# Kernel tuning notes

Measured on AMD Instinct MI355X. Metric: run time of the kernel, lower is better.

Reference implementation:

```python
import jax, jax.numpy as jnp
import numpy as np

B, D, N_CAT, S = 8192, 128, 8192, 4
EPS = 1e-12  # F.normalize eps


def setup_inputs() -> dict:
    key = jax.random.key(0)
    k1, k2, k3, k4 = jax.random.split(key, 4)
    return {
        "batch_x": jax.random.normal(k1, (B, D), dtype=jnp.float32),
        "cat": jax.random.normal(k2, (N_CAT, D), dtype=jnp.float32),
        "y": jax.random.uniform(k3, (N_CAT,), dtype=jnp.float32),
        "phi": jax.random.normal(k4, (S, D), dtype=jnp.float32) * (6.0 / (D + 1)) ** 0.5,  # xavier-ish scale
        "bias": jnp.zeros((1,), dtype=jnp.float32),
    }


def reference(batch_x, cat, y, phi, bias):
    # con[n, b] = cat[n] . batch_x[b]   -> [N_cat, B]
    con = cat @ batch_x.T
    # F.normalize(con, p=4, dim=0): divide each column by its 4-norm (clamped)
    norm4 = jnp.sum(jnp.abs(con) ** 4, axis=0, keepdims=True) ** 0.25
    con = con / jnp.maximum(norm4, EPS)
    con = jax.nn.softmax(con, axis=0)
    s = phi.shape[0]
    c = con.shape[0] // s
    psi = con.reshape(s, c, con.shape[1])      # source_size chunks of [C, B]
    y_r = y.reshape(s, c)                      # source_size chunks of labels
    theta = jnp.exp(batch_x @ phi.T).T         # [S, B], raw exp (theta/sum_src unused in original)
    # sum over sources and chunk rows of y[s,c] * psi[s,c,b] * theta[s,b]
    y_hat = jnp.einsum('sc,scb,sb->b', y_r, psi, theta) + bias
    return y_hat
```

## Files before the change

kernel.cpp:

```cpp
#include <hip/hip_runtime.h>
#include <hip/hip_bf16.h>
#include <math.h>

typedef __bf16 bf16x8 __attribute__((ext_vector_type(8)));
typedef float f32x4 __attribute__((ext_vector_type(4)));

namespace {
constexpr int BN   = 8192;
constexpr int DK   = 128;
constexpr int NCAT = 8192;
constexpr int SRC  = 4;
constexpr int RG   = 8;
constexpr int LDK  = 136;
}

__device__ __forceinline__ float4 ld4(const float* p) {
    return *reinterpret_cast<const float4*>(p);
}

__global__ __launch_bounds__(256) void k_convert(const float* __restrict__ in,
                                                 unsigned short* __restrict__ out,
                                                 int n8) {
    const int i = blockIdx.x * 256 + threadIdx.x;
    if (i >= n8) return;
    const float4 a = ld4(in + (size_t)i * 8);
    const float4 b = ld4(in + (size_t)i * 8 + 4);
    float vals[8] = {a.x, a.y, a.z, a.w, b.x, b.y, b.z, b.w};
    union { unsigned short u[8]; uint4 v; } o;
#pragma unroll
    for (int j = 0; j < 8; ++j) {
        __hip_bfloat16 h = __float2bfloat16(vals[j]);
        o.u[j] = *reinterpret_cast<unsigned short*>(&h);
    }
    *reinterpret_cast<uint4*>(&out[(size_t)i * 8]) = o.v;
}

template <int PASS>
__global__ __launch_bounds__(256, 2) void k_mfma_pass(
    const unsigned short* __restrict__ xb,
    const unsigned short* __restrict__ catb,
    const float* __restrict__ y,
    const float* __restrict__ inv_norm,
    const float* __restrict__ vmax,
    float* __restrict__ outA,
    float* __restrict__ outB) {
    __shared__ __align__(16) unsigned short As[128 * LDK];
    __shared__ __align__(16) unsigned short Bs[128 * LDK];
    __shared__ float ysh[128];
    __shared__ float redA[2][128];
    __shared__ float redB[2][128];

    const int t = threadIdx.x;
    const int colbase = blockIdx.x * 128;
    const int rowgrp = blockIdx.y;
    const int rowbase0 = rowgrp * 1024;

    const int wid = t >> 6;
    const int lane = t & 63;
    const int wr = wid >> 1;
    const int wc = wid & 1;
    const int lr = lane & 15;
    const int kb = lane >> 4;

#pragma unroll
    for (int q = t; q < 2048; q += 256) {
        const int c = q >> 4, kc = q & 15;
        *reinterpret_cast<uint4*>(&Bs[c * LDK + kc * 8]) =
            *reinterpret_cast<const uint4*>(&xb[(size_t)(colbase + c) * DK + kc * 8]);
    }

    float accA[4], accB[4];
    float inm[4], vmx4[4];
#pragma unroll
    for (int j = 0; j < 4; ++j) {
        accA[j] = 0.f;
        accB[j] = (PASS == 1) ? -3.0e38f : 0.f;
        if (PASS == 2) {
            const int col = colbase + wc * 64 + j * 16 + lr;
            inm[j] = inv_norm[col];
            vmx4[j] = vmax[col];
        }
    }

    for (int rt = 0; rt < 8; ++rt) {
        const int rowbase = rowbase0 + rt * 128;
        __syncthreads();
#pragma unroll
        for (int q = t; q < 2048; q += 256) {
            const int r = q >> 4, kc = q & 15;
            *reinterpret_cast<uint4*>(&As[r * LDK + kc * 8]) =
                *reinterpret_cast<const uint4*>(&catb[(size_t)(rowbase + r) * DK + kc * 8]);
        }
        if (PASS == 2 && t < 128) ysh[t] = y[rowbase + t];
        __syncthreads();

        f32x4 acc[4][4];
#pragma unroll
        for (int i = 0; i < 4; ++i)
#pragma unroll
            for (int j = 0; j < 4; ++j) acc[i][j] = (f32x4){0.f, 0.f, 0.f, 0.f};

#pragma unroll
        for (int kk = 0; kk < 4; ++kk) {
            bf16x8 a[4], b[4];
#pragma unroll
            for (int i = 0; i < 4; ++i)
                a[i] = *reinterpret_cast<const bf16x8*>(
                    &As[(wr * 64 + i * 16 + lr) * LDK + kk * 32 + kb * 8]);
#pragma unroll
            for (int j = 0; j < 4; ++j)
                b[j] = *reinterpret_cast<const bf16x8*>(
                    &Bs[(wc * 64 + j * 16 + lr) * LDK + kk * 32 + kb * 8]);
#pragma unroll
            for (int i = 0; i < 4; ++i)
#pragma unroll
                for (int j = 0; j < 4; ++j)
                    acc[i][j] = __builtin_amdgcn_mfma_f32_16x16x32_bf16(
                        a[i], b[j], acc[i][j], 0, 0, 0);
        }

        if (PASS == 1) {
#pragma unroll
            for (int i = 0; i < 4; ++i)
#pragma unroll
                for (int j = 0; j < 4; ++j)
#pragma unroll
                    for (int r = 0; r < 4; ++r) {
                        const float v = acc[i][j][r];
                        const float v2 = v * v;
                        accA[j] += v2 * v2;
                        accB[j] = fmaxf(accB[j], v);
                    }
        } else {
#pragma unroll
            for (int i = 0; i < 4; ++i)
#pragma unroll
                for (int r = 0; r < 4; ++r) {
                    const float yr = ysh[wr * 64 + i * 16 + kb * 4 + r];
#pragma unroll
                    for (int j = 0; j < 4; ++j) {
                        const float e = __expf(fmaf(acc[i][j][r], inm[j], -vmx4[j]));
                        accA[j] += e;
                        accB[j] += yr * e;
                    }
                }
        }
    }

#pragma unroll
    for (int j = 0; j < 4; ++j) {
        float a16 = __shfl_xor(accA[j], 16, 64);
        float b16 = __shfl_xor(accB[j], 16, 64);
        accA[j] += a16;
        accB[j] = (PASS == 1) ? fmaxf(accB[j], b16) : accB[j] + b16;
        float a32 = __shfl_xor(accA[j], 32, 64);
        float b32 = __shfl_xor(accB[j], 32, 64);
        accA[j] += a32;
        accB[j] = (PASS == 1) ? fmaxf(accB[j], b32) : accB[j] + b32;
    }

    if (lane < 16) {
#pragma unroll
        for (int j = 0; j < 4; ++j) {
            redA[wr][wc * 64 + j * 16 + lane] = accA[j];
            redB[wr][wc * 64 + j * 16 + lane] = accB[j];
        }
    }
    __syncthreads();
    if (t < 128) {
        const float a = redA[0][t] + redA[1][t];
        const float b = (PASS == 1) ? fmaxf(redB[0][t], redB[1][t])
                                    : redB[0][t] + redB[1][t];
        outA[(size_t)rowgrp * BN + colbase + t] = a;
        outB[(size_t)rowgrp * BN + colbase + t] = b;
    }
}

__global__ __launch_bounds__(256) void k_norm(const float* __restrict__ pp4,
                                              const float* __restrict__ pmax,
                                              float* __restrict__ inv_norm,
                                              float* __restrict__ vmax) {
    const int b = blockIdx.x * 256 + threadIdx.x;
    float sp = 0.f, sm = -3.0e38f;
#pragma unroll
    for (int r = 0; r < RG; ++r) {
        sp += pp4[r * BN + b];
        sm = fmaxf(sm, pmax[r * BN + b]);
    }
    float n4 = sqrtf(sqrtf(sp));
    n4 = fmaxf(n4, 1e-12f);
    const float inv = 1.0f / n4;
    inv_norm[b] = inv;
    vmax[b] = sm * inv;
}

__global__ __launch_bounds__(256) void k_final(const float* __restrict__ x,
                                               const float* __restrict__ phi,
                                               const float* __restrict__ pZ,
                                               const float* __restrict__ pW,
                                               const float* __restrict__ bias,
                                               float* __restrict__ out) {
    const int g = blockIdx.x * 256 + threadIdx.x;
    const int b = g >> 2, s = g & 3;
    float dot = 0.f;
#pragma unroll
    for (int k = 0; k < DK; k += 4) {
        const float4 xv = ld4(&x[(size_t)b * DK + k]);
        const float4 pv = ld4(&phi[s * DK + k]);
        dot += xv.x * pv.x + xv.y * pv.y + xv.z * pv.z + xv.w * pv.w;
    }
    const float W = pW[(size_t)(2 * s) * BN + b] + pW[(size_t)(2 * s + 1) * BN + b];
    float v = __expf(dot) * W;
    float Z = pZ[(size_t)(2 * s) * BN + b] + pZ[(size_t)(2 * s + 1) * BN + b];
    v += __shfl_xor(v, 1, 64);
    v += __shfl_xor(v, 2, 64);
    Z += __shfl_xor(Z, 1, 64);
    Z += __shfl_xor(Z, 2, 64);
    if (s == 0) out[b] = v / Z + bias[0];
}

extern "C" void kernel_launch(void* const* d_in, const int* in_sizes, int n_in,
                              void* d_out, int out_size, void* d_ws, size_t ws_size,
                              hipStream_t stream) {
    const float* x    = (const float*)d_in[0];
    const float* cat  = (const float*)d_in[1];
    const float* y    = (const float*)d_in[2];
    const float* phi  = (const float*)d_in[3];
    const float* bias = (const float*)d_in[4];
    float* out = (float*)d_out;

    char* ws = (char*)d_ws;
    unsigned short* xb   = (unsigned short*)ws;
    unsigned short* catb = xb + (size_t)BN * DK;
    float* pp4      = (float*)(catb + (size_t)NCAT * DK);
    float* pmax     = pp4 + (size_t)RG * BN;
    float* inv_norm = pmax + (size_t)RG * BN;
    float* vmax     = inv_norm + BN;
    float* pZ       = vmax + BN;
    float* pW       = pZ + (size_t)RG * BN;

    k_convert<<<(BN * DK / 8 + 255) / 256, 256, 0, stream>>>(x, xb, BN * DK / 8);
    k_convert<<<(NCAT * DK / 8 + 255) / 256, 256, 0, stream>>>(cat, catb, NCAT * DK / 8);
    k_mfma_pass<1><<<dim3(BN / 128, RG), 256, 0, stream>>>(xb, catb, y, nullptr, nullptr,
                                                           pp4, pmax);
    k_norm<<<BN / 256, 256, 0, stream>>>(pp4, pmax, inv_norm, vmax);
    k_mfma_pass<2><<<dim3(BN / 128, RG), 256, 0, stream>>>(xb, catb, y, inv_norm, vmax,
                                                           pZ, pW);
    k_final<<<BN * SRC / 256, 256, 0, stream>>>(x, phi, pZ, pW, bias, out);
}
```

Before: 73.76 us.

## Keep x tile in registers, fuse norm kernel and converts, use exp2

Loads the x (B operand) fragments straight into registers once per block instead of staging them in LDS, and doubles the cat row tile to 256 rows. The A tile alone then occupies LDS. Merges the two conversion launches into one and folds the separate norm kernel into the start of pass 2, with log2e pre-multiplied so exp2f replaces __expf. This cuts launch count, LDS traffic and LDS footprint, at the cost of extra registers for the persistent B fragments, which could affect the 2-blocks-per-CU occupancy.

```diff
diff --git a/kernel.cpp b/kernel.cpp
--- a/kernel.cpp
+++ b/kernel.cpp
@@ -12,41 +12,50 @@
 constexpr int SRC  = 4;
 constexpr int RG   = 8;
 constexpr int LDK  = 136;
+constexpr int RT   = 256;
+constexpr float LOG2E = 1.4426950408889634f;
 }
 
 __device__ __forceinline__ float4 ld4(const float* p) {
     return *reinterpret_cast<const float4*>(p);
 }
 
-__global__ __launch_bounds__(256) void k_convert(const float* __restrict__ in,
-                                                 unsigned short* __restrict__ out,
-                                                 int n8) {
+__global__ __launch_bounds__(256) void k_convert2(const float* __restrict__ x,
+                                                  const float* __restrict__ cat,
+                                                  unsigned short* __restrict__ xb,
+                                                  unsigned short* __restrict__ catb) {
     const int i = blockIdx.x * 256 + threadIdx.x;
-    if (i >= n8) return;
-    const float4 a = ld4(in + (size_t)i * 8);
-    const float4 b = ld4(in + (size_t)i * 8 + 4);
+    const int nx = BN * DK / 8;
+    const float* src;
+    unsigned short* dst;
+    int j;
+    if (i < nx) { src = x; dst = xb; j = i; }
+    else        { src = cat; dst = catb; j = i - nx; }
+    const float4 a = ld4(src + (size_t)j * 8);
+    const float4 b = ld4(src + (size_t)j * 8 + 4);
     float vals[8] = {a.x, a.y, a.z, a.w, b.x, b.y, b.z, b.w};
     union { unsigned short u[8]; uint4 v; } o;
 #pragma unroll
-    for (int j = 0; j < 8; ++j) {
-        __hip_bfloat16 h = __float2bfloat16(vals[j]);
-        o.u[j] = *reinterpret_cast<unsigned short*>(&h);
-    }
-    *reinterpret_cast<uint4*>(&out[(size_t)i * 8]) = o.v;
+    for (int q = 0; q < 8; ++q) {
+        __hip_bfloat16 h = __float2bfloat16(vals[q]);
+        o.u[q] = *reinterpret_cast<unsigned short*>(&h);
+    }
+    *reinterpret_cast<uint4*>(&dst[(size_t)j * 8]) = o.v;
 }
 
 template <int PASS>
-__global__ __launch_bounds__(256, 2) void k_mfma_pass(
+__global__ __launch_bounds__(256, 2) void k_pass(
     const unsigned short* __restrict__ xb,
     const unsigned short* __restrict__ catb,
     const float* __restrict__ y,
-    const float* __restrict__ inv_norm,
-    const float* __restrict__ vmax,
+    const float* __restrict__ pp4,
+    const float* __restrict__ pmax,
     float* __restrict__ outA,
     float* __restrict__ outB) {
-    __shared__ __align__(16) unsigned short As[128 * LDK];
-    __shared__ __align__(16) unsigned short Bs[128 * LDK];
-    __shared__ float ysh[128];
+    __shared__ __align__(16) unsigned short As[RT * LDK];
+    __shared__ float ysh[RT];
+    __shared__ float nsh[128];
+    __shared__ float msh[128];
     __shared__ float redA[2][128];
     __shared__ float redB[2][128];
 
@@ -62,88 +71,105 @@
     const int lr = lane & 15;
     const int kb = lane >> 4;
 
-#pragma unroll
-    for (int q = t; q < 2048; q += 256) {
-        const int c = q >> 4, kc = q & 15;
-        *reinterpret_cast<uint4*>(&Bs[c * LDK + kc * 8]) =
-            *reinterpret_cast<const uint4*>(&xb[(size_t)(colbase + c) * DK + kc * 8]);
+    if (PASS == 2 && t < 128) {
+        float sp = 0.f, sm = -3.0e38f;
+#pragma unroll
+        for (int r = 0; r < RG; ++r) {
+            sp += pp4[r * BN + colbase + t];
+            sm = fmaxf(sm, pmax[r * BN + colbase + t]);
+        }
+        const float n4 = fmaxf(sqrtf(sqrtf(sp)), 1e-12f);
+        const float L = LOG2E / n4;
+        nsh[t] = L;
+        msh[t] = sm * L;
+    }
+
+    bf16x8 Bf[4][4];
+#pragma unroll
+    for (int j = 0; j < 4; ++j)
+#pragma unroll
+        for (int kk = 0; kk < 4; ++kk)
+            Bf[j][kk] = *reinterpret_cast<const bf16x8*>(
+                &xb[(size_t)(colbase + wc * 64 + j * 16 + lr) * DK + kk * 32 + kb * 8]);
+
+    float inm[4], vmx4[4];
+    if (PASS == 2) {
+        __syncthreads();
+#pragma unroll
+        for (int j = 0; j < 4; ++j) {
+            inm[j] = nsh[wc * 64 + j * 16 + lr];
+            vmx4[j] = msh[wc * 64 + j * 16 + lr];
+        }
     }
 
     float accA[4], accB[4];
-    float inm[4], vmx4[4];
 #pragma unroll
     for (int j = 0; j < 4; ++j) {
         accA[j] = 0.f;
         accB[j] = (PASS == 1) ? -3.0e38f : 0.f;
-        if (PASS == 2) {
-            const int col = colbase + wc * 64 + j * 16 + lr;
-            inm[j] = inv_norm[col];
-            vmx4[j] = vmax[col];
-        }
-    }
-
-    for (int rt = 0; rt < 8; ++rt) {
-        const int rowbase = rowbase0 + rt * 128;
+    }
+
+    for (int rt0 = 0; rt0 < 1024; rt0 += RT) {
+        const int rowbase = rowbase0 + rt0;
         __syncthreads();
 #pragma unroll
-        for (int q = t; q < 2048; q += 256) {
+        for (int q = t; q < RT * 16; q += 256) {
             const int r = q >> 4, kc = q & 15;
             *reinterpret_cast<uint4*>(&As[r * LDK + kc * 8]) =
                 *reinterpret_cast<const uint4*>(&catb[(size_t)(rowbase + r) * DK + kc * 8]);
         }
-        if (PASS == 2 && t < 128) ysh[t] = y[rowbase + t];
+        if (PASS == 2) ysh[t] = y[rowbase + t];
         __syncthreads();
 
-        f32x4 acc[4][4];
-#pragma unroll
-        for (int i = 0; i < 4; ++i)
-#pragma unroll
-            for (int j = 0; j < 4; ++j) acc[i][j] = (f32x4){0.f, 0.f, 0.f, 0.f};
-
-#pragma unroll
-        for (int kk = 0; kk < 4; ++kk) {
-            bf16x8 a[4], b[4];
+#pragma unroll
+        for (int ch = 0; ch < 2; ++ch) {
+            f32x4 acc[4][4];
 #pragma unroll
             for (int i = 0; i < 4; ++i)
-                a[i] = *reinterpret_cast<const bf16x8*>(
-                    &As[(wr * 64 + i * 16 + lr) * LDK + kk * 32 + kb * 8]);
-#pragma unroll
-            for (int j = 0; j < 4; ++j)
-                b[j] = *reinterpret_cast<const bf16x8*>(
-                    &Bs[(wc * 64 + j * 16 + lr) * LDK + kk * 32 + kb * 8]);
-#pragma unroll
-            for (int i = 0; i < 4; ++i)
-#pragma unroll
-                for (int j = 0; j < 4; ++j)
-                    acc[i][j] = __builtin_amdgcn_mfma_f32_16x16x32_bf16(
-                        a[i], b[j], acc[i][j], 0, 0, 0);
-        }
-
-        if (PASS == 1) {
-#pragma unroll
-            for (int i = 0; i < 4; ++i)
-#pragma unroll
-                for (int j = 0; j < 4; ++j)
+#pragma unroll
+                for (int j = 0; j < 4; ++j) acc[i][j] = (f32x4){0.f, 0.f, 0.f, 0.f};
+
+#pragma unroll
+            for (int kk = 0; kk < 4; ++kk) {
+                bf16x8 a[4];
+#pragma unroll
+                for (int i = 0; i < 4; ++i)
+                    a[i] = *reinterpret_cast<const bf16x8*>(
+                        &As[(ch * 128 + wr * 64 + i * 16 + lr) * LDK + kk * 32 + kb * 8]);
+#pragma unroll
+                for (int i = 0; i < 4; ++i)
+#pragma unroll
+                    for (int j = 0; j < 4; ++j)
+                        acc[i][j] = __builtin_amdgcn_mfma_f32_16x16x32_bf16(
+                            a[i], Bf[j][kk], acc[i][j], 0, 0, 0);
+            }
+
+            if (PASS == 1) {
+#pragma unroll
+                for (int i = 0; i < 4; ++i)
+#pragma unroll
+                    for (int j = 0; j < 4; ++j)
+#pragma unroll
+                        for (int r = 0; r < 4; ++r) {
+                            const float v = acc[i][j][r];
+                            const float v2 = v * v;
+                            accA[j] = fmaf(v2, v2, accA[j]);
+                            accB[j] = fmaxf(accB[j], v);
+                        }
+            } else {
+#pragma unroll
+                for (int i = 0; i < 4; ++i)
 #pragma unroll
                     for (int r = 0; r < 4; ++r) {
-                        const float v = acc[i][j][r];
-                        const float v2 = v * v;
-                        accA[j] += v2 * v2;
-                        accB[j] = fmaxf(accB[j], v);
+                        const float yr = ysh[ch * 128 + wr * 64 + i * 16 + kb * 4 + r];
+#pragma unroll
+                        for (int j = 0; j < 4; ++j) {
+                            const float e = exp2f(fmaf(acc[i][j][r], inm[j], -vmx4[j]));
+                            accA[j] += e;
+                            accB[j] = fmaf(yr, e, accB[j]);
+                        }
                     }
-        } else {
-#pragma unroll
-            for (int i = 0; i < 4; ++i)
-#pragma unroll
-                for (int r = 0; r < 4; ++r) {
-                    const float yr = ysh[wr * 64 + i * 16 + kb * 4 + r];
-#pragma unroll
-                    for (int j = 0; j < 4; ++j) {
-                        const float e = __expf(fmaf(acc[i][j][r], inm[j], -vmx4[j]));
-                        accA[j] += e;
-                        accB[j] += yr * e;
-                    }
-                }
+            }
         }
     }
 
@@ -176,24 +202,6 @@
     }
 }
 
-__global__ __launch_bounds__(256) void k_norm(const float* __restrict__ pp4,
-                                              const float* __restrict__ pmax,
-                                              float* __restrict__ inv_norm,
-                                              float* __restrict__ vmax) {
-    const int b = blockIdx.x * 256 + threadIdx.x;
-    float sp = 0.f, sm = -3.0e38f;
-#pragma unroll
-    for (int r = 0; r < RG; ++r) {
-        sp += pp4[r * BN + b];
-        sm = fmaxf(sm, pmax[r * BN + b]);
-    }
-    float n4 = sqrtf(sqrtf(sp));
-    n4 = fmaxf(n4, 1e-12f);
-    const float inv = 1.0f / n4;
-    inv_norm[b] = inv;
-    vmax[b] = sm * inv;
-}
-
 __global__ __launch_bounds__(256) void k_final(const float* __restrict__ x,
                                                const float* __restrict__ phi,
                                                const float* __restrict__ pZ,
@@ -232,19 +240,14 @@
     char* ws = (char*)d_ws;
     unsigned short* xb   = (unsigned short*)ws;
     unsigned short* catb = xb + (size_t)BN * DK;
-    float* pp4      = (float*)(catb + (size_t)NCAT * DK);
-    float* pmax     = pp4 + (size_t)RG * BN;
-    float* inv_norm = pmax + (size_t)RG * BN;
-    float* vmax     = inv_norm + BN;
-    float* pZ       = vmax + BN;
-    float* pW       = pZ + (size_t)RG * BN;
-
-    k_convert<<<(BN * DK / 8 + 255) / 256, 256, 0, stream>>>(x, xb, BN * DK / 8);
-    k_convert<<<(NCAT * DK / 8 + 255) / 256, 256, 0, stream>>>(cat, catb, NCAT * DK / 8);
-    k_mfma_pass<1><<<dim3(BN / 128, RG), 256, 0, stream>>>(xb, catb, y, nullptr, nullptr,
-                                                           pp4, pmax);
-    k_norm<<<BN / 256, 256, 0, stream>>>(pp4, pmax, inv_norm, vmax);
-    k_mfma_pass<2><<<dim3(BN / 128, RG), 256, 0, stream>>>(xb, catb, y, inv_norm, vmax,
-                                                           pZ, pW);
+    float* pp4 = (float*)(catb + (size_t)NCAT * DK);
+    float* pmax = pp4 + (size_t)RG * BN;
+    float* pZ = pmax + (size_t)RG * BN;
+    float* pW = pZ + (size_t)RG * BN;
+
+    k_convert2<<<(BN * DK + NCAT * DK) / 8 / 256, 256, 0, stream>>>(x, cat, xb, catb);
+    k_pass<1><<<dim3(BN / 128, RG), 256, 0, stream>>>(xb, catb, y, nullptr, nullptr,
+                                                      pp4, pmax);
+    k_pass<2><<<dim3(BN / 128, RG), 256, 0, stream>>>(xb, catb, y, pp4, pmax, pZ, pW);
     k_final<<<BN * SRC / 256, 256, 0, stream>>>(x, phi, pZ, pW, bias, out);
 }
```

Result: slower. 81.74 us (+10.8%).
